# Performance work log

Measured on AMD Instinct MI355X. Metric: run time of the kernel, lower is better.

The kernel has to match this reference:

```python
import jax, jax.numpy as jnp
import numpy as np

EPS = 1e-5

def _layer_norm(x, w, b):
    mu = jnp.mean(x, axis=-1, keepdims=True)
    var = jnp.mean(jnp.square(x - mu), axis=-1, keepdims=True)
    return (x - mu) * jax.lax.rsqrt(var + EPS) * w + b

def setup_inputs() -> dict:
    key = jax.random.key(0)
    ks = jax.random.split(key, 4)
    B, S, H, D = 8, 2048, 8, 64
    E = H * D  # hidden_size = 512
    x = jax.random.normal(ks[0], (B * S, E), dtype=jnp.float32)
    w_uvqk = jax.random.normal(ks[1], (E, 4 * H * D), dtype=jnp.float32) * (E ** -0.5)
    b_uvqk = jax.random.normal(ks[2], (4 * H * D,), dtype=jnp.float32) * 0.02
    w_proj = jax.random.normal(ks[3], (H * D, E), dtype=jnp.float32) * ((H * D) ** -0.5)
    return {
        "x": x,
        "w_uvqk": w_uvqk,
        "b_uvqk": b_uvqk,
        "ln_in_w": jnp.ones((E,), jnp.float32),
        "ln_in_b": jnp.zeros((E,), jnp.float32),
        "ln_out_w": jnp.ones((H * D,), jnp.float32),
        "ln_out_b": jnp.zeros((H * D,), jnp.float32),
        "w_proj": w_proj,
        "batch_size": B,
        "max_seqlen": S,
        "num_targets": 64,
    }

def reference(x, w_uvqk, b_uvqk, ln_in_w, ln_in_b, ln_out_w, ln_out_b, w_proj,
              batch_size, max_seqlen, num_targets):
    B, S = batch_size, max_seqlen
    E = x.shape[-1]
    HD = w_proj.shape[0]          # num_heads * head_dim
    D = 64
    H = HD // D
    alpha = 1.0 / (D ** 0.5)

    # input layer norm
    xn = _layer_norm(x, ln_in_w, ln_in_b)                      # [T, E]
    # fused addmm + silu -> u, v, q, k
    mixed = jax.nn.silu(xn @ w_uvqk + b_uvqk)                  # [T, 4*H*D]
    u, v, q, k = jnp.split(mixed, 4, axis=-1)
    q = q.reshape(B, S, H, D)
    k = k.reshape(B, S, H, D)
    v = v.reshape(B, S, H, D)

    # HSTU silu attention: attn = silu(alpha * q k^T) / scaling_seqlen, masked
    scores = jnp.einsum("bshd,bthd->bhst", q, k) * alpha       # [B,H,S,S]
    attn = jax.nn.silu(scores) / jnp.float32(S)

    # causal mask + target mask: targets (last num_targets positions) are keys
    # only for themselves (target_group_size = 1)
    i = jnp.arange(S)[:, None]
    j = jnp.arange(S)[None, :]
    causal = j <= i
    key_is_history = j < (S - num_targets)
    mask = causal & (key_is_history | (i == j))                # [S,S]
    attn = jnp.where(mask[None, None], attn, 0.0)

    attn_out = jnp.einsum("bhst,bthd->bshd", attn, v)          # [B,S,H,D]
    attn_out = attn_out.reshape(B * S, HD)

    # ln_mul: u * layer_norm(attn_out)
    parallel = u * _layer_norm(attn_out, ln_out_w, ln_out_b)   # [T, HD]

    # residual projection
    out = parallel @ w_proj + x                                # [T, E]
    return out
```

## Files before the change

kernel.cpp:

```cpp
#include <hip/hip_runtime.h>
#include <hip/hip_bf16.h>

#define Bc 8
#define Sc 2048
#define Hc 8
#define Dc 64
#define Ec 512
#define NTc 64
#define Tc (Bc*Sc)
#define N1c (4*Hc*Dc)
#define HISTc (Sc - NTc)

typedef float f32x4 __attribute__((ext_vector_type(4)));
typedef __bf16 bf16x8 __attribute__((ext_vector_type(8)));
typedef short short8 __attribute__((ext_vector_type(8)));
typedef short s4v __attribute__((ext_vector_type(4)));

__device__ __forceinline__ unsigned short f2bf(float f){
  unsigned int u = __float_as_uint(f);
  u += 0x7fffu + ((u >> 16) & 1u);
  return (unsigned short)(u >> 16);
}
__device__ __forceinline__ float bf2f(unsigned short h){
  return __uint_as_float(((unsigned int)h) << 16);
}
__device__ __forceinline__ unsigned int pkbf(float a, float b){
  float2 f; f.x = a; f.y = b;
  __hip_bfloat162 h = __float22bfloat162_rn(f);
  unsigned int u;
  __builtin_memcpy(&u, &h, 4);
  return u;
}
__device__ __forceinline__ s4v pk4(float a, float b, float c, float d){
  uint2 u; u.x = pkbf(a, b); u.y = pkbf(c, d);
  return __builtin_bit_cast(s4v, u);
}
__device__ __forceinline__ float silu_f(float x){
  return x * __builtin_amdgcn_rcpf(1.f + __expf(-x));
}
__device__ __forceinline__ bf16x8 ldb8(const unsigned short* p){
  return __builtin_bit_cast(bf16x8, *(const short8*)p);
}
__device__ __forceinline__ f32x4 mfma16(bf16x8 a, bf16x8 b, f32x4 c){
  return __builtin_amdgcn_mfma_f32_16x16x32_bf16(a, b, c, 0, 0, 0);
}
__device__ __forceinline__ void gl_lds16(const void* g, void* l){
  __builtin_amdgcn_global_load_lds((const __attribute__((address_space(1))) unsigned int*)g,
                                   (__attribute__((address_space(3))) unsigned int*)l, 16, 0, 0);
}
__device__ __forceinline__ void pswap16(unsigned int &a, unsigned int &b){
  asm volatile("v_permlane16_swap_b32 %0, %1" : "+v"(a), "+v"(b));
}

__global__ __launch_bounds__(1024) void k_transpose_cast(const float* __restrict__ in,
                                                         unsigned short* __restrict__ out,
                                                         int R, int C){
  __shared__ float tile[32][33];
  int tx = threadIdx.x, ty = threadIdx.y;
  int c0 = blockIdx.x * 32, r0 = blockIdx.y * 32;
  tile[ty][tx] = in[(size_t)(r0 + ty) * C + c0 + tx];
  __syncthreads();
  out[(size_t)(c0 + ty) * R + r0 + tx] = f2bf(tile[tx][ty]);
}

__global__ __launch_bounds__(256) void k_ln_in(const float* __restrict__ x, const float* __restrict__ g,
                                               const float* __restrict__ b, unsigned short* __restrict__ xn){
  int lane = threadIdx.x & 63;
  int row = blockIdx.x * 4 + (threadIdx.x >> 6);
  const float* xr = x + (size_t)row * Ec + lane * 8;
  float4 v0 = *(const float4*)xr;
  float4 v1 = *(const float4*)(xr + 4);
  float vv[8] = {v0.x, v0.y, v0.z, v0.w, v1.x, v1.y, v1.z, v1.w};
  float s = 0.f, ss = 0.f;
  #pragma unroll
  for (int j = 0; j < 8; ++j){ s += vv[j]; ss += vv[j] * vv[j]; }
  #pragma unroll
  for (int m = 1; m < 64; m <<= 1){ s += __shfl_xor(s, m); ss += __shfl_xor(ss, m); }
  float mu = s * (1.f / Ec);
  float rs = rsqrtf(ss * (1.f / Ec) - mu * mu + 1e-5f);
  int c = lane * 8;
  float o[8];
  #pragma unroll
  for (int j = 0; j < 8; ++j) o[j] = (vv[j] - mu) * rs * g[c + j] + b[c + j];
  uint4 pk; pk.x = pkbf(o[0], o[1]); pk.y = pkbf(o[2], o[3]);
  pk.z = pkbf(o[4], o[5]); pk.w = pkbf(o[6], o[7]);
  *(uint4*)(xn + (size_t)row * Ec + c) = pk;
}

__global__ __launch_bounds__(256) void k_ln_mul(const unsigned short* __restrict__ att, const float* __restrict__ g,
                                                const float* __restrict__ b, const unsigned short* __restrict__ u,
                                                unsigned short* __restrict__ par){
  int lane = threadIdx.x & 63;
  int row = blockIdx.x * 4 + (threadIdx.x >> 6);
  short8 a8 = *(const short8*)(att + (size_t)row * Ec + lane * 8);
  short8 u8 = *(const short8*)(u + (size_t)row * Ec + lane * 8);
  float vv[8];
  #pragma unroll
  for (int j = 0; j < 8; ++j) vv[j] = bf2f((unsigned short)a8[j]);
  float s = 0.f, ss = 0.f;
  #pragma unroll
  for (int j = 0; j < 8; ++j){ s += vv[j]; ss += vv[j] * vv[j]; }
  #pragma unroll
  for (int m = 1; m < 64; m <<= 1){ s += __shfl_xor(s, m); ss += __shfl_xor(ss, m); }
  float mu = s * (1.f / Ec);
  float rs = rsqrtf(ss * (1.f / Ec) - mu * mu + 1e-5f);
  int c = lane * 8;
  float o[8];
  #pragma unroll
  for (int j = 0; j < 8; ++j){
    float uu = bf2f((unsigned short)u8[j]);
    o[j] = uu * ((vv[j] - mu) * rs * g[c + j] + b[c + j]);
  }
  uint4 pk; pk.x = pkbf(o[0], o[1]); pk.y = pkbf(o[2], o[3]);
  pk.z = pkbf(o[4], o[5]); pk.w = pkbf(o[6], o[7]);
  *(uint4*)(par + (size_t)row * Ec + c) = pk;
}

__global__ __launch_bounds__(256) void k_gemm_uvqk(const unsigned short* __restrict__ A,
                                                   const unsigned short* __restrict__ BT,
                                                   const float* __restrict__ bias,
                                                   unsigned short* __restrict__ u_out,
                                                   unsigned short* __restrict__ vT,
                                                   unsigned short* __restrict__ qb,
                                                   unsigned short* __restrict__ kb){
  __shared__ __align__(16) unsigned short As[2][128 * 32];
  __shared__ __align__(16) unsigned short Bs[2][128 * 32];
  int tid = threadIdx.x;
  int lane = tid & 63, w = tid >> 6;
  int lm = lane & 15, quad = lane >> 4;
  int wm = w & 1, wn = w >> 1;
  int bid = blockIdx.y * gridDim.x + blockIdx.x;
  int id2 = (bid & 7) * 256 + (bid >> 3);
  int n0 = (id2 & 15) << 7, m0 = (id2 >> 4) << 7;
  int cat = n0 >> 9;
  bool swp = (cat != 1);
  int xc = quad ^ ((lm >> 1) & 3);

  int r0s = tid >> 2, c0s = ((tid & 3) ^ ((r0s >> 1) & 3)) * 16;
  int r1s = r0s + 64;
  const char* saA0 = (const char*)(A  + (size_t)(m0 + r0s) * Ec) + c0s;
  const char* saA1 = (const char*)(A  + (size_t)(m0 + r1s) * Ec) + c0s;
  const char* saB0 = (const char*)(BT + (size_t)(n0 + r0s) * Ec) + c0s;
  const char* saB1 = (const char*)(BT + (size_t)(n0 + r1s) * Ec) + c0s;

  gl_lds16(saA0, (char*)As[0] + tid * 16);
  gl_lds16(saA1, (char*)As[0] + tid * 16 + 4096);
  gl_lds16(saB0, (char*)Bs[0] + tid * 16);
  gl_lds16(saB1, (char*)Bs[0] + tid * 16 + 4096);
  __syncthreads();

  f32x4 acc[4][4] = {};
  #pragma unroll 1
  for (int kt = 0; kt < 16; ++kt){
    int cur = kt & 1, nb = cur ^ 1;
    if (kt < 15){
      int k0 = (kt + 1) * 64;
      gl_lds16(saA0 + k0, (char*)As[nb] + tid * 16);
      gl_lds16(saA1 + k0, (char*)As[nb] + tid * 16 + 4096);
      gl_lds16(saB0 + k0, (char*)Bs[nb] + tid * 16);
      gl_lds16(saB1 + k0, (char*)Bs[nb] + tid * 16 + 4096);
    }
    bf16x8 af[4], bfr[4];
    #pragma unroll
    for (int s = 0; s < 4; ++s)
      af[s]  = ldb8(As[cur] + ((wm * 64 + s * 16 + lm) * 4 + xc) * 8);
    #pragma unroll
    for (int t = 0; t < 4; ++t)
      bfr[t] = ldb8(Bs[cur] + ((wn * 64 + t * 16 + lm) * 4 + xc) * 8);
    if (swp){
      #pragma unroll
      for (int s = 0; s < 4; ++s)
        #pragma unroll
        for (int t = 0; t < 4; ++t)
          acc[s][t] = mfma16(bfr[t], af[s], acc[s][t]);
    } else {
      #pragma unroll
      for (int s = 0; s < 4; ++s)
        #pragma unroll
        for (int t = 0; t < 4; ++t)
          acc[s][t] = mfma16(af[s], bfr[t], acc[s][t]);
    }
    __syncthreads();
  }

  if (cat == 1){
    #pragma unroll
    for (int t = 0; t < 4; ++t){
      int colg = n0 + wn * 64 + t * 16 + lm;
      float bv = bias[colg];
      int c = colg & 511, h = c >> 6, d = c & 63;
      #pragma unroll
      for (int s = 0; s < 4; ++s){
        int row = m0 + wm * 64 + s * 16 + quad * 4;
        int bb_ = row >> 11, sr = row & (Sc - 1);
        s4v pv = pk4(silu_f(acc[s][t][0] + bv), silu_f(acc[s][t][1] + bv),
                     silu_f(acc[s][t][2] + bv), silu_f(acc[s][t][3] + bv));
        *(s4v*)(vT + ((size_t)(bb_ * Hc + h) * Dc + d) * Sc + sr) = pv;
      }
    }
  } else {
    #pragma unroll
    for (int s = 0; s < 4; ++s){
      int row = m0 + wm * 64 + s * 16 + lm;
      int bb_ = row >> 11, sr = row & (Sc - 1);
      #pragma unroll
      for (int t = 0; t < 4; ++t){
        int colg = n0 + wn * 64 + t * 16 + quad * 4;
        float4 bv = *(const float4*)(bias + colg);
        float v0 = silu_f(acc[s][t][0] + bv.x);
        float v1 = silu_f(acc[s][t][1] + bv.y);
        float v2 = silu_f(acc[s][t][2] + bv.z);
        float v3 = silu_f(acc[s][t][3] + bv.w);
        int c = colg & 511, h = c >> 6, d = c & 63;
        if (cat == 0){
          *(s4v*)(u_out + (size_t)row * Ec + c) = pk4(v0, v1, v2, v3);
        } else if (cat == 2){
          *(s4v*)(qb + ((size_t)(bb_ * Hc + h) * Sc + sr) * Dc + d) =
            pk4(v0 * 0.125f, v1 * 0.125f, v2 * 0.125f, v3 * 0.125f);
        } else {
          *(s4v*)(kb + ((size_t)(bb_ * Hc + h) * Sc + sr) * Dc + d) = pk4(v0, v1, v2, v3);
        }
      }
    }
  }
}

__global__ __launch_bounds__(256) void k_attn(const unsigned short* __restrict__ qb,
                                              const unsigned short* __restrict__ kb,
                                              const unsigned short* __restrict__ vT,
                                              unsigned short* __restrict__ att){
  __shared__ __align__(16) unsigned short Kb[2][64 * 64];
  __shared__ __align__(16) unsigned short Vb[2][64 * 64];
  int tid = threadIdx.x;
  int lane = tid & 63, w = tid >> 6;
  int lm = lane & 15, quad = lane >> 4;
  int lmx = lm & 7;
  int bid = blockIdx.y * gridDim.x + blockIdx.x;
  int id2 = (bid & 7) * 256 + (bid >> 3);
  int bh = id2 >> 5;
  int qblk = 31 - (id2 & 31);
  int qrow = qblk * 64 + w * 16;
  int lastT = qblk;
  int ntiles = lastT + 1;

  const unsigned short* kbp = kb + (size_t)bh * Sc * Dc;
  const unsigned short* vbp = vT + (size_t)bh * Dc * Sc;
  const unsigned short* qp = qb + ((size_t)bh * Sc + qrow + lm) * Dc + quad * 8;
  bf16x8 qa0 = ldb8(qp), qa1 = ldb8(qp + 32);

  int r0s = tid >> 3, c0s = ((tid & 7) ^ (r0s & 7)) * 16;
  int r1s = (tid + 256) >> 3, c1s = (((tid + 256) & 7) ^ (r1s & 7)) * 16;
  const char* kS0 = (const char*)kbp + (size_t)r0s * 128 + c0s;
  const char* kS1 = (const char*)kbp + (size_t)r1s * 128 + c1s;
  const char* vS0 = (const char*)vbp + (size_t)r0s * (Sc * 2) + c0s;
  const char* vS1 = (const char*)vbp + (size_t)r1s * (Sc * 2) + c1s;

  {
    gl_lds16(kS0, (char*)Kb[0] + tid * 16);
    gl_lds16(kS1, (char*)Kb[0] + tid * 16 + 4096);
    gl_lds16(vS0, (char*)Vb[0] + tid * 16);
    gl_lds16(vS1, (char*)Vb[0] + tid * 16 + 4096);
  }
  __syncthreads();

  f32x4 o[4] = {};
  int qg = qrow + lm;
  int g = ((quad & 1) << 1) | (quad >> 1);
  int koff0 = lm * 64 + (quad ^ lmx) * 8;
  int koff1 = lm * 64 + (((quad + 4)) ^ lmx) * 8;
  int voff0 = lm * 64 + ((g ^ lmx)) * 8;
  int voff1 = lm * 64 + (((g + 4) ^ lmx)) * 8;

  auto step = [&](const unsigned short* Kc, const unsigned short* Vc,
                  char* dK, char* dV, int kt, bool do_stage){
    if (do_stage){
      gl_lds16(kS0 + (size_t)(kt + 1) * 8192, dK);
      gl_lds16(kS1 + (size_t)(kt + 1) * 8192, dK + 4096);
      gl_lds16(vS0 + (size_t)(kt + 1) * 128, dV);
      gl_lds16(vS1 + (size_t)(kt + 1) * 128, dV + 4096);
    }
    bool maskT = (kt == lastT);
    int key0 = kt * 64;
    unsigned int dlo[4], dhi[4];
    #pragma unroll
    for (int s = 0; s < 4; ++s){
      bf16x8 kf0 = ldb8(Kc + koff0 + s * 1024);
      bf16x8 kf1 = ldb8(Kc + koff1 + s * 1024);
      f32x4 sc = {0.f, 0.f, 0.f, 0.f};
      sc = mfma16(kf0, qa0, sc);
      sc = mfma16(kf1, qa1, sc);
      float p[4];
      if (maskT){
        #pragma unroll
        for (int r = 0; r < 4; ++r){
          int kg = key0 + s * 16 + quad * 4 + r;
          bool ok = (kg <= qg) && ((kg < HISTc) || (kg == qg));
          p[r] = ok ? silu_f(sc[r]) : 0.f;
        }
      } else {
        #pragma unroll
        for (int r = 0; r < 4; ++r) p[r] = silu_f(sc[r]);
      }
      dlo[s] = pkbf(p[0], p[1]);
      dhi[s] = pkbf(p[2], p[3]);
    }
    pswap16(dlo[0], dlo[1]); pswap16(dhi[0], dhi[1]);
    pswap16(dlo[2], dlo[3]); pswap16(dhi[2], dhi[3]);
    uint4 pa0u, pa1u;
    pa0u.x = dlo[0]; pa0u.y = dhi[0]; pa0u.z = dlo[1]; pa0u.w = dhi[1];
    pa1u.x = dlo[2]; pa1u.y = dhi[2]; pa1u.z = dlo[3]; pa1u.w = dhi[3];
    bf16x8 pa0 = __builtin_bit_cast(bf16x8, pa0u);
    bf16x8 pa1 = __builtin_bit_cast(bf16x8, pa1u);
    __builtin_amdgcn_s_setprio(1);
    #pragma unroll
    for (int t = 0; t < 4; ++t){
      bf16x8 vf0 = ldb8(Vc + voff0 + t * 1024);
      bf16x8 vf1 = ldb8(Vc + voff1 + t * 1024);
      o[t] = mfma16(pa0, vf0, o[t]);
      o[t] = mfma16(pa1, vf1, o[t]);
    }
    __builtin_amdgcn_s_setprio(0);
    __syncthreads();
  };

  int kt = 0;
  #pragma unroll 1
  for (; kt + 2 <= ntiles; kt += 2){
    step(Kb[0], Vb[0], (char*)Kb[1] + tid * 16, (char*)Vb[1] + tid * 16, kt, true);
    step(Kb[1], Vb[1], (char*)Kb[0] + tid * 16, (char*)Vb[0] + tid * 16, kt + 1, kt + 2 < ntiles);
  }
  if (kt < ntiles)
    step(Kb[0], Vb[0], (char*)Kb[1] + tid * 16, (char*)Vb[1] + tid * 16, kt, false);

  int bb_ = bh >> 3, hh = bh & 7;
  #pragma unroll
  for (int t = 0; t < 4; ++t){
    int d = t * 16 + lm;
    unsigned int p01 = pkbf(o[t][0] * (1.f / Sc), o[t][1] * (1.f / Sc));
    unsigned int p23 = pkbf(o[t][2] * (1.f / Sc), o[t][3] * (1.f / Sc));
    size_t base = ((size_t)(bb_ * Sc + qrow + quad * 4) * Hc + hh) * Dc + d;
    att[base]               = (unsigned short)p01;
    att[base + Hc * Dc]     = (unsigned short)(p01 >> 16);
    att[base + 2 * Hc * Dc] = (unsigned short)p23;
    att[base + 3 * Hc * Dc] = (unsigned short)(p23 >> 16);
  }
}

__global__ __launch_bounds__(256) void k_gemm_proj(const unsigned short* __restrict__ A,
                                                   const unsigned short* __restrict__ BT,
                                                   const float* __restrict__ x,
                                                   float* __restrict__ out){
  __shared__ __align__(16) unsigned short As[2][128 * 32];
  __shared__ __align__(16) unsigned short Bs[2][128 * 32];
  int tid = threadIdx.x;
  int lane = tid & 63, w = tid >> 6;
  int lm = lane & 15, quad = lane >> 4;
  int wm = w & 1, wn = w >> 1;
  int bid = blockIdx.y * gridDim.x + blockIdx.x;
  int id2 = (bid & 7) * 64 + (bid >> 3);
  int n0 = (id2 & 3) << 7, m0 = (id2 >> 2) << 7;
  int xc = quad ^ ((lm >> 1) & 3);

  int r0s = tid >> 2, c0s = ((tid & 3) ^ ((r0s >> 1) & 3)) * 16;
  int r1s = r0s + 64;
  const char* saA0 = (const char*)(A  + (size_t)(m0 + r0s) * Ec) + c0s;
  const char* saA1 = (const char*)(A  + (size_t)(m0 + r1s) * Ec) + c0s;
  const char* saB0 = (const char*)(BT + (size_t)(n0 + r0s) * Ec) + c0s;
  const char* saB1 = (const char*)(BT + (size_t)(n0 + r1s) * Ec) + c0s;

  gl_lds16(saA0, (char*)As[0] + tid * 16);
  gl_lds16(saA1, (char*)As[0] + tid * 16 + 4096);
  gl_lds16(saB0, (char*)Bs[0] + tid * 16);
  gl_lds16(saB1, (char*)Bs[0] + tid * 16 + 4096);
  __syncthreads();

  f32x4 acc[4][4] = {};
  #pragma unroll 1
  for (int kt = 0; kt < 16; ++kt){
    int cur = kt & 1, nb = cur ^ 1;
    if (kt < 15){
      int k0 = (kt + 1) * 64;
      gl_lds16(saA0 + k0, (char*)As[nb] + tid * 16);
      gl_lds16(saA1 + k0, (char*)As[nb] + tid * 16 + 4096);
      gl_lds16(saB0 + k0, (char*)Bs[nb] + tid * 16);
      gl_lds16(saB1 + k0, (char*)Bs[nb] + tid * 16 + 4096);
    }
    bf16x8 af[4], bfr[4];
    #pragma unroll
    for (int s = 0; s < 4; ++s)
      af[s]  = ldb8(As[cur] + ((wm * 64 + s * 16 + lm) * 4 + xc) * 8);
    #pragma unroll
    for (int t = 0; t < 4; ++t)
      bfr[t] = ldb8(Bs[cur] + ((wn * 64 + t * 16 + lm) * 4 + xc) * 8);
    #pragma unroll
    for (int s = 0; s < 4; ++s)
      #pragma unroll
      for (int t = 0; t < 4; ++t)
        acc[s][t] = mfma16(bfr[t], af[s], acc[s][t]);
    __syncthreads();
  }

  #pragma unroll
  for (int s = 0; s < 4; ++s){
    int row = m0 + wm * 64 + s * 16 + lm;
    #pragma unroll
    for (int t = 0; t < 4; ++t){
      int col = n0 + wn * 64 + t * 16 + quad * 4;
      float4 xr = *(const float4*)(x + (size_t)row * Ec + col);
      float4 o4 = {acc[s][t][0] + xr.x, acc[s][t][1] + xr.y,
                   acc[s][t][2] + xr.z, acc[s][t][3] + xr.w};
      *(float4*)(out + (size_t)row * Ec + col) = o4;
    }
  }
}

extern "C" void kernel_launch(void* const* d_in, const int* in_sizes, int n_in,
                              void* d_out, int out_size, void* d_ws, size_t ws_size,
                              hipStream_t stream){
  (void)in_sizes; (void)n_in; (void)out_size; (void)ws_size;
  const float* x        = (const float*)d_in[0];
  const float* w_uvqk   = (const float*)d_in[1];
  const float* b_uvqk   = (const float*)d_in[2];
  const float* ln_in_w  = (const float*)d_in[3];
  const float* ln_in_b  = (const float*)d_in[4];
  const float* ln_out_w = (const float*)d_in[5];
  const float* ln_out_b = (const float*)d_in[6];
  const float* w_proj   = (const float*)d_in[7];
  float* out = (float*)d_out;

  char* ws = (char*)d_ws;
  unsigned short* xn  = (unsigned short*)(ws + 0);
  unsigned short* wuT = (unsigned short*)(ws + 16777216);
  unsigned short* wpT = (unsigned short*)(ws + 18874368);
  unsigned short* ub  = (unsigned short*)(ws + 19398656);
  unsigned short* qbf = (unsigned short*)(ws + 52953088);
  unsigned short* kbf = (unsigned short*)(ws + 69730304);
  unsigned short* vTt = (unsigned short*)(ws + 86507520);
  unsigned short* att = (unsigned short*)(ws + 103284736);

  dim3 tb(32, 32);
  k_transpose_cast<<<dim3(N1c / 32, Ec / 32), tb, 0, stream>>>(w_uvqk, wuT, Ec, N1c);
  k_transpose_cast<<<dim3(Ec / 32, Ec / 32), tb, 0, stream>>>(w_proj, wpT, Ec, Ec);
  k_ln_in<<<Tc / 4, 256, 0, stream>>>(x, ln_in_w, ln_in_b, xn);
  k_gemm_uvqk<<<dim3(N1c / 128, Tc / 128), 256, 0, stream>>>(xn, wuT, b_uvqk, ub, vTt, qbf, kbf);
  k_attn<<<dim3(Bc * Hc, Sc / 64), 256, 0, stream>>>(qbf, kbf, vTt, att);
  k_ln_mul<<<Tc / 4, 256, 0, stream>>>(att, ln_out_w, ln_out_b, ub, xn);
  k_gemm_proj<<<dim3(Ec / 128, Tc / 128), 256, 0, stream>>>(xn, wpT, x, out);
}
```

Measured before the change: 285.9 us.

## Enlarge attention query tile to 128 rows with two row groups per wave

Each attention block now processes 128 query rows instead of 64, and each wave handles two 16-row groups that share the same K and V fragments loaded from LDS. This halves the number of K/V tile loads per query row and improves MFMA-to-LDS-read ratio. Waves whose rows end before the final key tile skip compute on that tile. The trade-offs are more registers per thread, half as many blocks (possible occupancy and tail imbalance), and some idle waves on the diagonal tile.

```diff
diff --git a/kernel.cpp b/kernel.cpp
--- a/kernel.cpp
+++ b/kernel.cpp
@@ -236,17 +236,18 @@
   int lm = lane & 15, quad = lane >> 4;
   int lmx = lm & 7;
   int bid = blockIdx.y * gridDim.x + blockIdx.x;
-  int id2 = (bid & 7) * 256 + (bid >> 3);
-  int bh = id2 >> 5;
-  int qblk = 31 - (id2 & 31);
-  int qrow = qblk * 64 + w * 16;
-  int lastT = qblk;
-  int ntiles = lastT + 1;
+  int id2 = (bid & 7) * 128 + (bid >> 3);
+  int bh = id2 >> 4;
+  int qblk = 15 - (id2 & 15);
+  int qrow = qblk * 128 + w * 32;
+  int lastTw = 2 * qblk + (w >> 1);
+  int ntiles = 2 * qblk + 2;
 
   const unsigned short* kbp = kb + (size_t)bh * Sc * Dc;
   const unsigned short* vbp = vT + (size_t)bh * Dc * Sc;
   const unsigned short* qp = qb + ((size_t)bh * Sc + qrow + lm) * Dc + quad * 8;
-  bf16x8 qa0 = ldb8(qp), qa1 = ldb8(qp + 32);
+  bf16x8 qa00 = ldb8(qp),           qa01 = ldb8(qp + 32);
+  bf16x8 qa10 = ldb8(qp + 16 * Dc), qa11 = ldb8(qp + 16 * Dc + 32);
 
   int r0s = tid >> 3, c0s = ((tid & 7) ^ (r0s & 7)) * 16;
   int r1s = (tid + 256) >> 3, c1s = (((tid + 256) & 7) ^ (r1s & 7)) * 16;
@@ -263,8 +264,8 @@
   }
   __syncthreads();
 
-  f32x4 o[4] = {};
-  int qg = qrow + lm;
+  f32x4 o[2][4] = {};
+  int qg0 = qrow + lm, qg1 = qrow + 16 + lm;
   int g = ((quad & 1) << 1) | (quad >> 1);
   int koff0 = lm * 64 + (quad ^ lmx) * 8;
   int koff1 = lm * 64 + (((quad + 4)) ^ lmx) * 8;
@@ -279,47 +280,58 @@
       gl_lds16(vS0 + (size_t)(kt + 1) * 128, dV);
       gl_lds16(vS1 + (size_t)(kt + 1) * 128, dV + 4096);
     }
-    bool maskT = (kt == lastT);
-    int key0 = kt * 64;
-    unsigned int dlo[4], dhi[4];
-    #pragma unroll
-    for (int s = 0; s < 4; ++s){
-      bf16x8 kf0 = ldb8(Kc + koff0 + s * 1024);
-      bf16x8 kf1 = ldb8(Kc + koff1 + s * 1024);
-      f32x4 sc = {0.f, 0.f, 0.f, 0.f};
-      sc = mfma16(kf0, qa0, sc);
-      sc = mfma16(kf1, qa1, sc);
-      float p[4];
-      if (maskT){
-        #pragma unroll
-        for (int r = 0; r < 4; ++r){
-          int kg = key0 + s * 16 + quad * 4 + r;
-          bool ok = (kg <= qg) && ((kg < HISTc) || (kg == qg));
-          p[r] = ok ? silu_f(sc[r]) : 0.f;
+    if (kt <= lastTw){
+      bool maskT = (kt == lastTw);
+      int key0 = kt * 64;
+      unsigned int dloA[4], dhiA[4], dloB[4], dhiB[4];
+      #pragma unroll
+      for (int s = 0; s < 4; ++s){
+        bf16x8 kf0 = ldb8(Kc + koff0 + s * 1024);
+        bf16x8 kf1 = ldb8(Kc + koff1 + s * 1024);
+        f32x4 scA = {0.f, 0.f, 0.f, 0.f}, scB = {0.f, 0.f, 0.f, 0.f};
+        scA = mfma16(kf0, qa00, scA); scA = mfma16(kf1, qa01, scA);
+        scB = mfma16(kf0, qa10, scB); scB = mfma16(kf1, qa11, scB);
+        float pA[4], pB[4];
+        if (maskT){
+          #pragma unroll
+          for (int r = 0; r < 4; ++r){
+            int kg = key0 + s * 16 + quad * 4 + r;
+            bool okA = (kg <= qg0) && ((kg < HISTc) || (kg == qg0));
+            bool okB = (kg <= qg1) && ((kg < HISTc) || (kg == qg1));
+            pA[r] = okA ? silu_f(scA[r]) : 0.f;
+            pB[r] = okB ? silu_f(scB[r]) : 0.f;
+          }
+        } else {
+          #pragma unroll
+          for (int r = 0; r < 4; ++r){ pA[r] = silu_f(scA[r]); pB[r] = silu_f(scB[r]); }
         }
-      } else {
-        #pragma unroll
-        for (int r = 0; r < 4; ++r) p[r] = silu_f(sc[r]);
+        dloA[s] = pkbf(pA[0], pA[1]); dhiA[s] = pkbf(pA[2], pA[3]);
+        dloB[s] = pkbf(pB[0], pB[1]); dhiB[s] = pkbf(pB[2], pB[3]);
       }
-      dlo[s] = pkbf(p[0], p[1]);
-      dhi[s] = pkbf(p[2], p[3]);
-    }
-    pswap16(dlo[0], dlo[1]); pswap16(dhi[0], dhi[1]);
-    pswap16(dlo[2], dlo[3]); pswap16(dhi[2], dhi[3]);
-    uint4 pa0u, pa1u;
-    pa0u.x = dlo[0]; pa0u.y = dhi[0]; pa0u.z = dlo[1]; pa0u.w = dhi[1];
-    pa1u.x = dlo[2]; pa1u.y = dhi[2]; pa1u.z = dlo[3]; pa1u.w = dhi[3];
-    bf16x8 pa0 = __builtin_bit_cast(bf16x8, pa0u);
-    bf16x8 pa1 = __builtin_bit_cast(bf16x8, pa1u);
-    __builtin_amdgcn_s_setprio(1);
-    #pragma unroll
-    for (int t = 0; t < 4; ++t){
-      bf16x8 vf0 = ldb8(Vc + voff0 + t * 1024);
-      bf16x8 vf1 = ldb8(Vc + voff1 + t * 1024);
-      o[t] = mfma16(pa0, vf0, o[t]);
-      o[t] = mfma16(pa1, vf1, o[t]);
-    }
-    __builtin_amdgcn_s_setprio(0);
+      pswap16(dloA[0], dloA[1]); pswap16(dhiA[0], dhiA[1]);
+      pswap16(dloA[2], dloA[3]); pswap16(dhiA[2], dhiA[3]);
+      pswap16(dloB[0], dloB[1]); pswap16(dhiB[0], dhiB[1]);
+      pswap16(dloB[2], dloB[3]); pswap16(dhiB[2], dhiB[3]);
+      uint4 u0A = {dloA[0], dhiA[0], dloA[1], dhiA[1]};
+      uint4 u1A = {dloA[2], dhiA[2], dloA[3], dhiA[3]};
+      uint4 u0B = {dloB[0], dhiB[0], dloB[1], dhiB[1]};
+      uint4 u1B = {dloB[2], dhiB[2], dloB[3], dhiB[3]};
+      bf16x8 pa0A = __builtin_bit_cast(bf16x8, u0A);
+      bf16x8 pa1A = __builtin_bit_cast(bf16x8, u1A);
+      bf16x8 pa0B = __builtin_bit_cast(bf16x8, u0B);
+      bf16x8 pa1B = __builtin_bit_cast(bf16x8, u1B);
+      __builtin_amdgcn_s_setprio(1);
+      #pragma unroll
+      for (int t = 0; t < 4; ++t){
+        bf16x8 vf0 = ldb8(Vc + voff0 + t * 1024);
+        bf16x8 vf1 = ldb8(Vc + voff1 + t * 1024);
+        o[0][t] = mfma16(pa0A, vf0, o[0][t]);
+        o[0][t] = mfma16(pa1A, vf1, o[0][t]);
+        o[1][t] = mfma16(pa0B, vf0, o[1][t]);
+        o[1][t] = mfma16(pa1B, vf1, o[1][t]);
+      }
+      __builtin_amdgcn_s_setprio(0);
+    }
     __syncthreads();
   };
 
@@ -334,15 +346,18 @@
 
   int bb_ = bh >> 3, hh = bh & 7;
   #pragma unroll
-  for (int t = 0; t < 4; ++t){
-    int d = t * 16 + lm;
-    unsigned int p01 = pkbf(o[t][0] * (1.f / Sc), o[t][1] * (1.f / Sc));
-    unsigned int p23 = pkbf(o[t][2] * (1.f / Sc), o[t][3] * (1.f / Sc));
-    size_t base = ((size_t)(bb_ * Sc + qrow + quad * 4) * Hc + hh) * Dc + d;
-    att[base]               = (unsigned short)p01;
-    att[base + Hc * Dc]     = (unsigned short)(p01 >> 16);
-    att[base + 2 * Hc * Dc] = (unsigned short)p23;
-    att[base + 3 * Hc * Dc] = (unsigned short)(p23 >> 16);
+  for (int rg = 0; rg < 2; ++rg){
+    #pragma unroll
+    for (int t = 0; t < 4; ++t){
+      int d = t * 16 + lm;
+      unsigned int p01 = pkbf(o[rg][t][0] * (1.f / Sc), o[rg][t][1] * (1.f / Sc));
+      unsigned int p23 = pkbf(o[rg][t][2] * (1.f / Sc), o[rg][t][3] * (1.f / Sc));
+      size_t base = ((size_t)(bb_ * Sc + qrow + rg * 16 + quad * 4) * Hc + hh) * Dc + d;
+      att[base]               = (unsigned short)p01;
+      att[base + Hc * Dc]     = (unsigned short)(p01 >> 16);
+      att[base + 2 * Hc * Dc] = (unsigned short)p23;
+      att[base + 3 * Hc * Dc] = (unsigned short)(p23 >> 16);
+    }
   }
 }
 
@@ -443,7 +458,7 @@
   k_transpose_cast<<<dim3(Ec / 32, Ec / 32), tb, 0, stream>>>(w_proj, wpT, Ec, Ec);
   k_ln_in<<<Tc / 4, 256, 0, stream>>>(x, ln_in_w, ln_in_b, xn);
   k_gemm_uvqk<<<dim3(N1c / 128, Tc / 128), 256, 0, stream>>>(xn, wuT, b_uvqk, ub, vTt, qbf, kbf);
-  k_attn<<<dim3(Bc * Hc, Sc / 64), 256, 0, stream>>>(qbf, kbf, vTt, att);
+  k_attn<<<dim3(Bc * Hc, Sc / 128), 256, 0, stream>>>(qbf, kbf, vTt, att);
   k_ln_mul<<<Tc / 4, 256, 0, stream>>>(att, ln_out_w, ln_out_b, ub, xn);
   k_gemm_proj<<<dim3(Ec / 128, Tc / 128), 256, 0, stream>>>(xn, wpT, x, out);
 }
```

Result: slower. 298.9 us (+4.6%).

## Load K/V fragments directly from global memory in attention, dropping LDS staging

Applied to the files above, without the earlier changes.

Removes the double-buffered LDS staging of K and V tiles (global-to-LDS async loads plus a block barrier per tile) and has each wave load its MFMA fragments straight from global memory/cache. This eliminates __syncthreads and LDS traffic, letting the four waves run independently. The cost is that each of the four waves separately fetches the same K/V data, relying on L1/L2 hits, and the V loads are strided across rows of length Sc.

```diff
diff --git a/kernel.cpp b/kernel.cpp
--- a/kernel.cpp
+++ b/kernel.cpp
@@ -229,12 +229,9 @@
                                               const unsigned short* __restrict__ kb,
                                               const unsigned short* __restrict__ vT,
                                               unsigned short* __restrict__ att){
-  __shared__ __align__(16) unsigned short Kb[2][64 * 64];
-  __shared__ __align__(16) unsigned short Vb[2][64 * 64];
   int tid = threadIdx.x;
   int lane = tid & 63, w = tid >> 6;
   int lm = lane & 15, quad = lane >> 4;
-  int lmx = lm & 7;
   int bid = blockIdx.y * gridDim.x + blockIdx.x;
   int id2 = (bid & 7) * 256 + (bid >> 3);
   int bh = id2 >> 5;
@@ -248,47 +245,30 @@
   const unsigned short* qp = qb + ((size_t)bh * Sc + qrow + lm) * Dc + quad * 8;
   bf16x8 qa0 = ldb8(qp), qa1 = ldb8(qp + 32);
 
-  int r0s = tid >> 3, c0s = ((tid & 7) ^ (r0s & 7)) * 16;
-  int r1s = (tid + 256) >> 3, c1s = (((tid + 256) & 7) ^ (r1s & 7)) * 16;
-  const char* kS0 = (const char*)kbp + (size_t)r0s * 128 + c0s;
-  const char* kS1 = (const char*)kbp + (size_t)r1s * 128 + c1s;
-  const char* vS0 = (const char*)vbp + (size_t)r0s * (Sc * 2) + c0s;
-  const char* vS1 = (const char*)vbp + (size_t)r1s * (Sc * 2) + c1s;
-
-  {
-    gl_lds16(kS0, (char*)Kb[0] + tid * 16);
-    gl_lds16(kS1, (char*)Kb[0] + tid * 16 + 4096);
-    gl_lds16(vS0, (char*)Vb[0] + tid * 16);
-    gl_lds16(vS1, (char*)Vb[0] + tid * 16 + 4096);
-  }
-  __syncthreads();
-
   f32x4 o[4] = {};
   int qg = qrow + lm;
   int g = ((quad & 1) << 1) | (quad >> 1);
-  int koff0 = lm * 64 + (quad ^ lmx) * 8;
-  int koff1 = lm * 64 + (((quad + 4)) ^ lmx) * 8;
-  int voff0 = lm * 64 + ((g ^ lmx)) * 8;
-  int voff1 = lm * 64 + (((g + 4) ^ lmx)) * 8;
-
-  auto step = [&](const unsigned short* Kc, const unsigned short* Vc,
-                  char* dK, char* dV, int kt, bool do_stage){
-    if (do_stage){
-      gl_lds16(kS0 + (size_t)(kt + 1) * 8192, dK);
-      gl_lds16(kS1 + (size_t)(kt + 1) * 8192, dK + 4096);
-      gl_lds16(vS0 + (size_t)(kt + 1) * 128, dV);
-      gl_lds16(vS1 + (size_t)(kt + 1) * 128, dV + 4096);
-    }
+  const unsigned short* kB  = kbp + lm * Dc + quad * 8;
+  const unsigned short* vB0 = vbp + (size_t)lm * Sc + g * 8;
+  const unsigned short* vB1 = vbp + (size_t)lm * Sc + (g + 4) * 8;
+
+  #pragma unroll 2
+  for (int kt = 0; kt < ntiles; ++kt){
     bool maskT = (kt == lastT);
     int key0 = kt * 64;
+    const unsigned short* Kt = kB + kt * 4096;
+    bf16x8 kf0[4], kf1[4];
+    #pragma unroll
+    for (int s = 0; s < 4; ++s){
+      kf0[s] = ldb8(Kt + s * 1024);
+      kf1[s] = ldb8(Kt + s * 1024 + 32);
+    }
     unsigned int dlo[4], dhi[4];
     #pragma unroll
     for (int s = 0; s < 4; ++s){
-      bf16x8 kf0 = ldb8(Kc + koff0 + s * 1024);
-      bf16x8 kf1 = ldb8(Kc + koff1 + s * 1024);
       f32x4 sc = {0.f, 0.f, 0.f, 0.f};
-      sc = mfma16(kf0, qa0, sc);
-      sc = mfma16(kf1, qa1, sc);
+      sc = mfma16(kf0[s], qa0, sc);
+      sc = mfma16(kf1[s], qa1, sc);
       float p[4];
       if (maskT){
         #pragma unroll
@@ -311,26 +291,18 @@
     pa1u.x = dlo[2]; pa1u.y = dhi[2]; pa1u.z = dlo[3]; pa1u.w = dhi[3];
     bf16x8 pa0 = __builtin_bit_cast(bf16x8, pa0u);
     bf16x8 pa1 = __builtin_bit_cast(bf16x8, pa1u);
+    const unsigned short* Vt0 = vB0 + key0;
+    const unsigned short* Vt1 = vB1 + key0;
     __builtin_amdgcn_s_setprio(1);
     #pragma unroll
     for (int t = 0; t < 4; ++t){
-      bf16x8 vf0 = ldb8(Vc + voff0 + t * 1024);
-      bf16x8 vf1 = ldb8(Vc + voff1 + t * 1024);
+      bf16x8 vf0 = ldb8(Vt0 + (size_t)t * 16 * Sc);
+      bf16x8 vf1 = ldb8(Vt1 + (size_t)t * 16 * Sc);
       o[t] = mfma16(pa0, vf0, o[t]);
       o[t] = mfma16(pa1, vf1, o[t]);
     }
     __builtin_amdgcn_s_setprio(0);
-    __syncthreads();
-  };
-
-  int kt = 0;
-  #pragma unroll 1
-  for (; kt + 2 <= ntiles; kt += 2){
-    step(Kb[0], Vb[0], (char*)Kb[1] + tid * 16, (char*)Vb[1] + tid * 16, kt, true);
-    step(Kb[1], Vb[1], (char*)Kb[0] + tid * 16, (char*)Vb[0] + tid * 16, kt + 1, kt + 2 < ntiles);
-  }
-  if (kt < ntiles)
-    step(Kb[0], Vb[0], (char*)Kb[1] + tid * 16, (char*)Vb[1] + tid * 16, kt, false);
+  }
 
   int bb_ = bh >> 3, hh = bh & 7;
   #pragma unroll
```

Result: slower. 521.0 us (+82.2%).
